# Kernel optimization log

Measured on AMD Instinct MI355X. Metric: run time of the kernel, lower is better.

The kernel has to match this reference:

```python
import jax, jax.numpy as jnp
import numpy as np

NUM_HEADS = 8
D_CONV = 4
NORMALIZER = 16.0
LN_EPS = 1e-5


def setup_inputs() -> dict:
    key = jax.random.key(0)
    ks = jax.random.split(key, 9)
    B, L, E = 4, 2048, 1024
    dk = E // 2
    return {
        "x": jax.random.normal(ks[0], (B, L, E), jnp.float32),
        "conv_w": jax.random.normal(ks[1], (E, D_CONV), jnp.float32) * 0.3,
        "wq": jax.random.normal(ks[2], (E, dk), jnp.float32) * 0.02,
        "wkg": jax.random.normal(ks[3], (E, dk), jnp.float32) * 0.02,
        "wv": jax.random.normal(ks[4], (E, E), jnp.float32) * 0.02,
        "wg": jax.random.normal(ks[5], (E, E), jnp.float32) * 0.02,
        "bg": jax.random.normal(ks[6], (E,), jnp.float32) * 0.02,
        "wout": jax.random.normal(ks[7], (E, E), jnp.float32) * 0.02,
        "aug_balance": jax.random.normal(ks[8], (dk,), jnp.float32) * 0.1,
    }


def _causal_dwconv_silu(x, w):
    # x: [B, L, E]; w: [E, W] depthwise kernel. Causal: left-pad W-1 zeros.
    xt = jnp.transpose(x, (0, 2, 1))  # [B, E, L]
    y = jax.lax.conv_general_dilated(
        xt, w[:, None, :], window_strides=(1,), padding=[(w.shape[1] - 1, 0)],
        feature_group_count=x.shape[-1], dimension_numbers=("NCH", "OIH", "NCH"))
    return jnp.transpose(jax.nn.silu(y), (0, 2, 1))  # [B, L, E]


def _gla(q, k, v, gk, scale):
    # Gated linear attention recurrence (fused_chunk_gla math):
    #   S_t = S_{t-1} * exp(gk_t)[:, None] + k_t (outer) v_t
    #   o_t = (scale * q_t) @ S_t
    # q, k, gk: [B,H,L,Dk]; v: [B,H,L,Dv]
    B, H, L, Dk = q.shape
    Dv = v.shape[-1]

    def step(S, inp):
        qt, kt, vt, gt = inp  # [B,H,Dk], [B,H,Dk], [B,H,Dv], [B,H,Dk]
        S = S * jnp.exp(gt)[..., None] + kt[..., None] * vt[..., None, :]
        ot = jnp.einsum("bhk,bhkv->bhv", qt * scale, S)
        return S, ot

    mv = lambda a: jnp.moveaxis(a, 2, 0)  # L to leading axis for scan
    S0 = jnp.zeros((B, H, Dk, Dv), q.dtype)
    _, o = jax.lax.scan(step, S0, (mv(q), mv(k), mv(v), mv(gk)))
    return jnp.moveaxis(o, 0, 2)  # [B,H,L,Dv]


def reference(x, conv_w, wq, wkg, wv, wg, bg, wout, aug_balance):
    B, L, E = x.shape
    H = NUM_HEADS
    xc = _causal_dwconv_silu(x, conv_w)
    q = xc @ wq            # [B,L,dk]
    kg = xc @ wkg          # [B,L,dk]
    v = xc @ wv            # [B,L,E]
    g = xc @ wg + bg       # [B,L,E]

    gk = jax.nn.log_sigmoid(kg) / NORMALIZER
    k = 1.0 - jnp.exp(gk)

    dkh = q.shape[-1] // H  # key_dim per head
    to_heads = lambda t: t.reshape(B, L, H, -1).transpose(0, 2, 1, 3)
    qh, kh, vh, gkh = to_heads(q), to_heads(k), to_heads(v), to_heads(gk)

    scale = dkh ** -0.5
    o = _gla(qh, kh, vh, gkh, scale)  # [B,H,L,head_dim]

    # Augmented term: aug_w[b,h,l] = sum_d q[b,h,l,d] * aug[h,d] * k[b,h,l,d]
    aug = aug_balance.reshape(H, dkh)
    aug_w = jnp.einsum("bhld,hd,bhld->bhl", qh, aug, kh)
    o = o + jax.nn.sigmoid(aug_w[..., None] * vh)

    # LayerNorm over head_dim, no affine
    mu = o.mean(-1, keepdims=True)
    var = o.var(-1, keepdims=True)
    o = (o - mu) * jax.lax.rsqrt(var + LN_EPS)

    o = o.transpose(0, 2, 1, 3).reshape(B, L, E)
    return (jax.nn.silu(g) * o) @ wout
```

## Files before the change

### kernel.cpp

```cpp
#include <hip/hip_runtime.h>
#include <stdint.h>

typedef unsigned short u16;
typedef unsigned int u32;
typedef __attribute__((ext_vector_type(4))) float f32x4;
typedef __attribute__((ext_vector_type(8))) short short8;
typedef __attribute__((ext_vector_type(8))) _Float16 f16x8;

#define H 8
#define LSEQ 2048
#define E 1024
#define DK 512
#define DVH 128
#define DKH 64
#define NCHUNK 32
#define MROWS 8192
#define LN_EPS 1e-5f

static __device__ __forceinline__ float bf2f(u16 u) {
    union { float f; u32 i; } v; v.i = ((u32)u) << 16; return v.f;
}
static __device__ __forceinline__ u16 f2bf(float f) {
    union { float f; u32 i; } v; v.f = f;
    u32 r = v.i + 0x7FFFu + ((v.i >> 16) & 1u);
    return (u16)(r >> 16);
}

__global__ __launch_bounds__(256) void k_conv(const float* __restrict__ x,
                                              const float* __restrict__ cw,
                                              u16* __restrict__ xc) {
    const int l0 = blockIdx.x * 64;
    const int c  = blockIdx.y * 256 + threadIdx.x;
    const int b  = blockIdx.z;
    const f32x4 w = *(const f32x4*)(cw + c * 4);
    const float* base = x + (size_t)b * LSEQ * E + c;
    u16* ob = xc + (size_t)b * LSEQ * E + c;
    float x3 = (l0 >= 3) ? base[(size_t)(l0 - 3) * E] : 0.f;
    float x2 = (l0 >= 2) ? base[(size_t)(l0 - 2) * E] : 0.f;
    float x1 = (l0 >= 1) ? base[(size_t)(l0 - 1) * E] : 0.f;
#pragma unroll 8
    for (int r = 0; r < 64; r++) {
        const float x0 = base[(size_t)(l0 + r) * E];
        float a = x3 * w[0];
        a = fmaf(x2, w[1], a);
        a = fmaf(x1, w[2], a);
        a = fmaf(x0, w[3], a);
        const float s = a / (1.f + __expf(-a));
        ob[(size_t)(l0 + r) * E] = f2bf(s);
        x3 = x2; x2 = x1; x1 = x0;
    }
}

__global__ __launch_bounds__(256) void k_transpose_all(const float* __restrict__ wq,
                                                       const float* __restrict__ wkg,
                                                       const float* __restrict__ wv,
                                                       const float* __restrict__ wg,
                                                       const float* __restrict__ wout,
                                                       u16* __restrict__ wcat,
                                                       u16* __restrict__ woutT) {
    __shared__ float tile[32][33];
    const int z = blockIdx.z;
    const float* src; u16* dst; int Ncols;
    if (z == 0)      { src = wq;   dst = wcat;                        Ncols = 512; }
    else if (z == 1) { src = wkg;  dst = wcat + (size_t)512 * 1024;   Ncols = 512; }
    else if (z == 2) { src = wv;   dst = wcat + (size_t)1024 * 1024;  Ncols = 1024; }
    else if (z == 3) { src = wg;   dst = wcat + (size_t)2048 * 1024;  Ncols = 1024; }
    else             { src = wout; dst = woutT;                       Ncols = 1024; }
    const int n0 = blockIdx.x * 32, k0 = blockIdx.y * 32;
    if (n0 >= Ncols) return;
    const int K = 1024;
    const int tx = threadIdx.x & 31, ty = threadIdx.x >> 5;
#pragma unroll
    for (int p = 0; p < 4; p++) {
        const int r = p * 8 + ty;
        tile[r][tx] = src[(size_t)(k0 + r) * Ncols + n0 + tx];
    }
    __syncthreads();
#pragma unroll
    for (int p = 0; p < 4; p++) {
        const int rn = p * 8 + ty;
        dst[(size_t)(n0 + rn) * K + k0 + tx] = f2bf(tile[tx][rn]);
    }
}

__global__ __launch_bounds__(512, 1) void k_gemm0(const u16* __restrict__ A,
                                                  const u16* __restrict__ Bt,
                                                  u16* __restrict__ oQ, u16* __restrict__ oKG,
                                                  u16* __restrict__ oV, u16* __restrict__ oSG,
                                                  const float* __restrict__ bg) {
    const int K = 1024;
    __shared__ __align__(16) u16 smem[3][16384];
    const int tid = threadIdx.x;
    const int lane = tid & 63, wv = tid >> 6;
    const int wm = wv >> 2, wn = wv & 3;

    const int id = blockIdx.x;
    const int local = id >> 3;
    const int bx = ((id & 7) << 2) | (local & 3);
    const int by = local >> 2;

    const size_t rowBase = (size_t)bx * 256;
    const size_t colBase = (size_t)by * 256;

    auto stage = [&](int hh, int sl) {
        u16* slotA = &smem[sl][0];
        u16* slotB = &smem[sl][8192];
        const u16* gA = A + rowBase * K + hh * 32;
        const u16* gB = Bt + colBase * K + hh * 32;
#pragma unroll
        for (int i = 0; i < 2; i++) {
            const int u = i * 512 + wv * 64 + lane;
            const int row = u >> 2;
            const int sg = (lane & 3) ^ ((row >> 1) & 3);
            __builtin_amdgcn_global_load_lds(
                (const __attribute__((address_space(1))) void*)(gA + (size_t)row * K + sg * 8),
                (__attribute__((address_space(3))) void*)(slotA + (i * 512 + wv * 64) * 8), 16, 0, 0);
        }
#pragma unroll
        for (int i = 0; i < 2; i++) {
            const int u = i * 512 + wv * 64 + lane;
            const int row = u >> 2;
            const int sg = (lane & 3) ^ ((row >> 1) & 3);
            __builtin_amdgcn_global_load_lds(
                (const __attribute__((address_space(1))) void*)(gB + (size_t)row * K + sg * 8),
                (__attribute__((address_space(3))) void*)(slotB + (i * 512 + wv * 64) * 8), 16, 0, 0);
        }
    };

    f32x4 acc[8][4];
#pragma unroll
    for (int m = 0; m < 8; m++)
#pragma unroll
        for (int n = 0; n < 4; n++) acc[m][n] = (f32x4){0.f, 0.f, 0.f, 0.f};

    const int rsub = lane & 15;
    const int cgl = lane >> 4;

    stage(0, 0); stage(1, 1);

    const int NT2 = K >> 5;
    int sl = 0;
    for (int h = 0; h < NT2; h++) {
        if (h + 1 < NT2) asm volatile("s_waitcnt vmcnt(4)" ::: "memory");
        else             asm volatile("s_waitcnt vmcnt(0)" ::: "memory");
        asm volatile("s_barrier" ::: "memory");
        const u16* As = &smem[sl][0];
        const u16* Bs = &smem[sl][8192];
        short8 bfr[4];
#pragma unroll
        for (int ni = 0; ni < 4; ni++) {
            const int row = wn * 64 + ni * 16 + rsub;
            const int g = cgl ^ ((row >> 1) & 3);
            bfr[ni] = *(const short8*)(Bs + row * 32 + g * 8);
        }
        if (h + 2 < NT2) stage(h + 2, (sl + 2) % 3);
        __builtin_amdgcn_s_setprio(1);
#pragma unroll
        for (int mi = 0; mi < 8; mi++) {
            const int row = wm * 128 + mi * 16 + rsub;
            const int g = cgl ^ ((row >> 1) & 3);
            const short8 af = *(const short8*)(As + row * 32 + g * 8);
#pragma unroll
            for (int ni = 0; ni < 4; ni++)
                acc[mi][ni] = __builtin_amdgcn_mfma_f32_16x16x32_bf16(af, bfr[ni], acc[mi][ni], 0, 0, 0);
        }
        __builtin_amdgcn_s_setprio(0);
        sl = (sl + 1) % 3;
    }

    const int r0 = (lane >> 4) * 4;
    u16* lds = &smem[0][0];
    const int cbase = (int)colBase;
    u16* seg; int stride; int c0;
    if (cbase < 512)       { seg = oQ;  stride = 512;  c0 = cbase; }
    else if (cbase < 1024) { seg = oKG; stride = 512;  c0 = cbase - 512; }
    else if (cbase < 2048) { seg = oV;  stride = 1024; c0 = cbase - 1024; }
    else                   { seg = oSG; stride = 1024; c0 = cbase - 2048; }
    const bool isSG = (cbase >= 2048);
#pragma unroll
    for (int p = 0; p < 2; p++) {
        asm volatile("s_barrier" ::: "memory");
        if (wm == p) {
#pragma unroll
            for (int ni = 0; ni < 4; ni++) {
                const int lcol = wn * 64 + ni * 16 + rsub;
                const float bgv = isSG ? bg[cbase - 2048 + lcol] : 0.f;
#pragma unroll
                for (int mi = 0; mi < 8; mi++) {
#pragma unroll
                    for (int r = 0; r < 4; r++) {
                        const int lrow = mi * 16 + r0 + r;
                        float val = acc[mi][ni][r];
                        if (isSG) { const float y = val + bgv; val = y / (1.f + __expf(-y)); }
                        lds[lrow * 256 + lcol] = f2bf(val);
                    }
                }
            }
        }
        asm volatile("s_barrier" ::: "memory");
#pragma unroll
        for (int i = 0; i < 8; i++) {
            const int unit = i * 512 + tid;
            const int row = unit >> 5, u = unit & 31;
            const uint4 vv = *(const uint4*)(lds + row * 256 + u * 8);
            *(uint4*)(seg + (rowBase + p * 128 + row) * (size_t)stride + c0 + u * 8) = vv;
        }
    }
}

__global__ __launch_bounds__(512, 1) void k_gemm1(const u16* __restrict__ A,
                                                  const u16* __restrict__ Bt,
                                                  float* __restrict__ oF) {
    const int K = 1024, N = 1024;
    __shared__ __align__(16) u16 smem[4][12288];
    const int tid = threadIdx.x;
    const int lane = tid & 63, wv = tid >> 6;
    const int wm = wv >> 1, wn = wv & 1;

    const int id = blockIdx.y * gridDim.x + blockIdx.x;
    const int bx = ((id & 7) << 2) | ((id >> 3) & 3);
    const int by = id >> 5;

    const size_t rowBase = (size_t)bx * 256;
    const size_t colBase = (size_t)by * 128;

    auto stageA = [&](int hh) {
        u16* slotA = &smem[hh & 3][0];
        const u16* g = A + rowBase * K + hh * 32;
#pragma unroll
        for (int i = 0; i < 2; i++) {
            const int r = i * 128 + wv * 16 + (lane >> 2);
            const int sg = (lane & 3) ^ ((r >> 1) & 3);
            __builtin_amdgcn_global_load_lds(
                (const __attribute__((address_space(1))) void*)(g + (size_t)r * K + sg * 8),
                (__attribute__((address_space(3))) void*)(slotA + i * 4096 + wv * 512), 16, 0, 0);
        }
    };
    auto stageB = [&](int hh) {
        u16* slotB = &smem[hh & 3][8192];
        const u16* g = Bt + colBase * K + hh * 32;
        const int r = wv * 16 + (lane >> 2);
        const int sg = (lane & 3) ^ ((r >> 1) & 3);
        __builtin_amdgcn_global_load_lds(
            (const __attribute__((address_space(1))) void*)(g + (size_t)r * K + sg * 8),
            (__attribute__((address_space(3))) void*)(slotB + wv * 512), 16, 0, 0);
    };

    f32x4 acc[4][4];
#pragma unroll
    for (int m = 0; m < 4; m++)
#pragma unroll
        for (int n = 0; n < 4; n++) acc[m][n] = (f32x4){0.f, 0.f, 0.f, 0.f};

    const int rsub = lane & 15;
    const int cgl = lane >> 4;

    stageA(0); stageB(0);
    stageA(1); stageB(1);
    stageA(2); stageB(2);

    const int NT2 = K >> 5;
    for (int h = 0; h < NT2; h++) {
        const int rem = NT2 - 1 - h;
        if (rem >= 2)      asm volatile("s_waitcnt vmcnt(6)" ::: "memory");
        else if (rem == 1) asm volatile("s_waitcnt vmcnt(3)" ::: "memory");
        else               asm volatile("s_waitcnt vmcnt(0)" ::: "memory");
        asm volatile("s_barrier" ::: "memory");
        const u16* As = &smem[h & 3][0];
        const u16* Bs = As + 8192;
        short8 af[4], bfr[4];
#pragma unroll
        for (int mi = 0; mi < 4; mi++) {
            const int row = wm * 64 + mi * 16 + rsub;
            const int g = cgl ^ ((row >> 1) & 3);
            af[mi] = *(const short8*)(As + row * 32 + g * 8);
        }
#pragma unroll
        for (int ni = 0; ni < 4; ni++) {
            const int row = wn * 64 + ni * 16 + rsub;
            const int g = cgl ^ ((row >> 1) & 3);
            bfr[ni] = *(const short8*)(Bs + row * 32 + g * 8);
        }
        if (h + 3 < NT2) { stageA(h + 3); stageB(h + 3); }
        __builtin_amdgcn_s_setprio(1);
#pragma unroll
        for (int mi = 0; mi < 4; mi++)
#pragma unroll
            for (int ni = 0; ni < 4; ni++)
                acc[mi][ni] = __builtin_amdgcn_mfma_f32_16x16x32_bf16(af[mi], bfr[ni], acc[mi][ni], 0, 0, 0);
        __builtin_amdgcn_s_setprio(0);
    }

    const int r0 = (lane >> 4) * 4;
#pragma unroll
    for (int mi = 0; mi < 4; mi++)
#pragma unroll
        for (int ni = 0; ni < 4; ni++) {
            const size_t col = colBase + wn * 64 + ni * 16 + rsub;
#pragma unroll
            for (int r = 0; r < 4; r++) {
                const size_t row = rowBase + wm * 64 + mi * 16 + r0 + r;
                oF[row * (size_t)N + col] = acc[mi][ni][r];
            }
        }
}

__global__ __launch_bounds__(256) void k_gla1(const u16* __restrict__ q,
                                              const u16* __restrict__ kg,
                                              const u16* __restrict__ v,
                                              const float* __restrict__ aug,
                                              u16* __restrict__ qt,
                                              u16* __restrict__ obuf,
                                              float* __restrict__ Sd,
                                              float* __restrict__ Dc,
                                              float* __restrict__ augw) {
    __shared__ __align__(16) float    s_f[64][68];
    __shared__ __align__(16) _Float16 s_q[64][72];
    __shared__ __align__(16) _Float16 s_k[64][72];
    __shared__ __align__(16) _Float16 s_kT[64][72];
    __shared__ __align__(16) _Float16 s_a[64][72];
    __shared__ __align__(16) _Float16 s_vT[128][72];
    const int c = blockIdx.x, bh = blockIdx.y;
    const int b = bh >> 3, h = bh & 7;
    const int tid = threadIdx.x;
    const size_t rowBase = (size_t)b * LSEQ + c * 64;
    const size_t sdBase = (size_t)bh * NCHUNK + c;

    const int tA = tid >> 2, g4 = tid & 3;
    uint4 qr0, qr1;
    {
        const int d0 = g4 * 16;
        const u16* kp = kg + (rowBase + tA) * DK + h * 64 + d0;
        const uint4 k0 = *(const uint4*)kp;
        const uint4 k1 = *(const uint4*)(kp + 8);
        const u16 kv[16] = {
            (u16)(k0.x & 0xffff), (u16)(k0.x >> 16), (u16)(k0.y & 0xffff), (u16)(k0.y >> 16),
            (u16)(k0.z & 0xffff), (u16)(k0.z >> 16), (u16)(k0.w & 0xffff), (u16)(k0.w >> 16),
            (u16)(k1.x & 0xffff), (u16)(k1.x >> 16), (u16)(k1.y & 0xffff), (u16)(k1.y >> 16),
            (u16)(k1.z & 0xffff), (u16)(k1.z >> 16), (u16)(k1.w & 0xffff), (u16)(k1.w >> 16) };
#pragma unroll
        for (int j = 0; j < 16; j++) {
            const float xk = bf2f(kv[j]);
            const float ls = fminf(xk, 0.f) - __logf(1.f + __expf(-fabsf(xk)));
            s_f[tA][d0 + j] = ls * (1.f / 16.f);
        }
        const u16* qp = q + (rowBase + tA) * DK + h * 64 + d0;
        qr0 = *(const uint4*)qp;
        qr1 = *(const uint4*)(qp + 8);

        const int dv0 = g4 * 32;
        const u16* vp = v + (rowBase + tA) * E + h * 128 + dv0;
#pragma unroll
        for (int j8 = 0; j8 < 32; j8 += 8) {
            const uint4 u = *(const uint4*)(vp + j8);
            s_vT[dv0 + j8 + 0][tA] = (_Float16)bf2f((u16)(u.x & 0xffff));
            s_vT[dv0 + j8 + 1][tA] = (_Float16)bf2f((u16)(u.x >> 16));
            s_vT[dv0 + j8 + 2][tA] = (_Float16)bf2f((u16)(u.y & 0xffff));
            s_vT[dv0 + j8 + 3][tA] = (_Float16)bf2f((u16)(u.y >> 16));
            s_vT[dv0 + j8 + 4][tA] = (_Float16)bf2f((u16)(u.z & 0xffff));
            s_vT[dv0 + j8 + 5][tA] = (_Float16)bf2f((u16)(u.z >> 16));
            s_vT[dv0 + j8 + 6][tA] = (_Float16)bf2f((u16)(u.w & 0xffff));
            s_vT[dv0 + j8 + 7][tA] = (_Float16)bf2f((u16)(u.w >> 16));
        }
    }
    __syncthreads();

    {
        const int d = tid >> 2, qseg = tid & 3;
        float part = 0.f;
#pragma unroll
        for (int j = 0; j < 16; j++) part += s_f[qseg * 16 + j][d];
        float incl = part;
        const float u1 = __shfl_up(incl, 1, 4); if (qseg >= 1) incl += u1;
        const float u2 = __shfl_up(incl, 2, 4); if (qseg >= 2) incl += u2;
        float run = incl - part;
#pragma unroll
        for (int j = 0; j < 16; j++) {
            const int t = qseg * 16 + j;
            const float g = s_f[t][d];
            run += g;
            const float kk = 1.f - __expf(g);
            const float ktil = kk * __expf(-run);
            s_k[t][d] = (_Float16)ktil;
            s_kT[d][t] = (_Float16)ktil;
            s_a[t][d] = (_Float16)kk;
            s_f[t][d] = run;
        }
    }
    __syncthreads();

    {
        const int t = tA, d0 = g4 * 16;
        const u16 qv16[16] = {
            (u16)(qr0.x & 0xffff), (u16)(qr0.x >> 16), (u16)(qr0.y & 0xffff), (u16)(qr0.y >> 16),
            (u16)(qr0.z & 0xffff), (u16)(qr0.z >> 16), (u16)(qr0.w & 0xffff), (u16)(qr0.w >> 16),
            (u16)(qr1.x & 0xffff), (u16)(qr1.x >> 16), (u16)(qr1.y & 0xffff), (u16)(qr1.y >> 16),
            (u16)(qr1.z & 0xffff), (u16)(qr1.z >> 16), (u16)(qr1.w & 0xffff), (u16)(qr1.w >> 16) };
        float qv[16];
        float augp = 0.f;
#pragma unroll
        for (int j = 0; j < 16; j++) {
            const int d = d0 + j;
            const float qraw = bf2f(qv16[j]);
            const float L = s_f[t][d];
            const float kk = (float)s_a[t][d];
            const float qtv = qraw * __expf(L) * 0.125f;
            s_q[t][d] = (_Float16)qtv;
            qv[j] = qtv;
            augp = fmaf(qraw * aug[h * 64 + d], kk, augp);
        }
        u16* qto = qt + (rowBase + t) * DK + h * 64 + d0;
#pragma unroll
        for (int j8 = 0; j8 < 16; j8 += 8) {
            uint4 u;
            u.x = (u32)f2bf(qv[j8 + 0]) | ((u32)f2bf(qv[j8 + 1]) << 16);
            u.y = (u32)f2bf(qv[j8 + 2]) | ((u32)f2bf(qv[j8 + 3]) << 16);
            u.z = (u32)f2bf(qv[j8 + 4]) | ((u32)f2bf(qv[j8 + 5]) << 16);
            u.w = (u32)f2bf(qv[j8 + 6]) | ((u32)f2bf(qv[j8 + 7]) << 16);
            *(uint4*)(qto + j8) = u;
        }
        augp += __shfl_xor(augp, 1);
        augp += __shfl_xor(augp, 2);
        if ((tid & 3) == 0) augw[(size_t)bh * LSEQ + c * 64 + t] = augp;
    }
    __syncthreads();

    const int wv = tid >> 6, lane = tid & 63;
    const int rsub = lane & 15, kq8 = (lane >> 4) * 8, r0 = (lane >> 4) * 4;
    {
#pragma unroll
        for (int si = 0; si < 4; si++) {
            if (si <= wv) {
                f32x4 acc = (f32x4){0.f, 0.f, 0.f, 0.f};
#pragma unroll
                for (int kk = 0; kk < 2; kk++) {
                    const f16x8 af = *(const f16x8*)&s_q[wv * 16 + rsub][kk * 32 + kq8];
                    const f16x8 bf = *(const f16x8*)&s_k[si * 16 + rsub][kk * 32 + kq8];
                    acc = __builtin_amdgcn_mfma_f32_16x16x32_f16(af, bf, acc, 0, 0, 0);
                }
                const int scol = si * 16 + rsub;
#pragma unroll
                for (int r = 0; r < 4; r++) {
                    const int trow = wv * 16 + r0 + r;
                    const float val = (scol <= trow) ? acc[r] : 0.f;
                    s_a[trow][scol] = (_Float16)val;
                }
            } else {
#pragma unroll
                for (int r = 0; r < 4; r++)
                    s_a[wv * 16 + r0 + r][si * 16 + rsub] = (_Float16)0.f;
            }
        }
    }
    __syncthreads();

    {
        f32x4 oacc[8];
#pragma unroll
        for (int n = 0; n < 8; n++) oacc[n] = (f32x4){0.f, 0.f, 0.f, 0.f};
        const f16x8 a0 = *(const f16x8*)&s_a[wv * 16 + rsub][kq8];
        const f16x8 a1 = *(const f16x8*)&s_a[wv * 16 + rsub][32 + kq8];
#pragma unroll
        for (int n = 0; n < 8; n++) {
            const f16x8 b0 = *(const f16x8*)&s_vT[n * 16 + rsub][kq8];
            const f16x8 b1 = *(const f16x8*)&s_vT[n * 16 + rsub][32 + kq8];
            oacc[n] = __builtin_amdgcn_mfma_f32_16x16x32_f16(a0, b0, oacc[n], 0, 0, 0);
            oacc[n] = __builtin_amdgcn_mfma_f32_16x16x32_f16(a1, b1, oacc[n], 0, 0, 0);
        }
        u16* ob = obuf + ((size_t)bh * LSEQ + c * 64) * DVH;
#pragma unroll
        for (int n = 0; n < 8; n++) {
            const int dv = n * 16 + rsub;
#pragma unroll
            for (int r = 0; r < 4; r++) {
                const int trow = wv * 16 + r0 + r;
                ob[(size_t)trow * DVH + dv] = f2bf(oacc[n][r]);
            }
        }
    }

    {
        f32x4 sacc[8];
#pragma unroll
        for (int n = 0; n < 8; n++) sacc[n] = (f32x4){0.f, 0.f, 0.f, 0.f};
        const f16x8 a0 = *(const f16x8*)&s_kT[wv * 16 + rsub][kq8];
        const f16x8 a1 = *(const f16x8*)&s_kT[wv * 16 + rsub][32 + kq8];
#pragma unroll
        for (int n = 0; n < 8; n++) {
            const f16x8 b0 = *(const f16x8*)&s_vT[n * 16 + rsub][kq8];
            const f16x8 b1 = *(const f16x8*)&s_vT[n * 16 + rsub][32 + kq8];
            sacc[n] = __builtin_amdgcn_mfma_f32_16x16x32_f16(a0, b0, sacc[n], 0, 0, 0);
            sacc[n] = __builtin_amdgcn_mfma_f32_16x16x32_f16(a1, b1, sacc[n], 0, 0, 0);
        }
        float dend[4];
#pragma unroll
        for (int r = 0; r < 4; r++) dend[r] = __expf(s_f[63][wv * 16 + r0 + r]);
#pragma unroll
        for (int n = 0; n < 8; n++) {
            const int dv = n * 16 + rsub;
#pragma unroll
            for (int r = 0; r < 4; r++) {
                const int d = wv * 16 + r0 + r;
                Sd[(sdBase * DKH + d) * DVH + dv] = sacc[n][r] * dend[r];
            }
        }
        if (rsub == 0) {
#pragma unroll
            for (int r = 0; r < 4; r++) {
                const int d = wv * 16 + r0 + r;
                Dc[sdBase * DKH + d] = dend[r];
            }
        }
    }
}

__global__ __launch_bounds__(256) void k_gla2(const float* __restrict__ Sd,
                                              u16* __restrict__ Ss,
                                              const float* __restrict__ Dc) {
    const int cid = blockIdx.x * 256 + threadIdx.x;
    const int bh = cid >> 13;
    const int e = cid & 8191;
    const int d = e >> 7;
    float run = 0.f;
    const size_t base = (size_t)bh * NCHUNK * 8192 + e;
    for (int c = 0; c < NCHUNK; c++) {
        const size_t idx = base + (size_t)c * 8192;
        const float dl = Sd[idx];
        Ss[idx] = f2bf(run);
        run = fmaf(Dc[((size_t)bh * NCHUNK + c) * DKH + d], run, dl);
    }
}

__global__ __launch_bounds__(256) void k_gla3(const u16* __restrict__ qt,
                                              const u16* __restrict__ v,
                                              const u16* __restrict__ sg,
                                              const u16* __restrict__ obuf,
                                              const u16* __restrict__ Ss,
                                              const float* __restrict__ augw,
                                              u16* __restrict__ a2) {
    __shared__ __align__(16) _Float16 s_ST[128][72];
    __shared__ __align__(16) _Float16 s_qr[64][72];
    __shared__ __align__(16) float    s_O2[64][132];
    const int c = blockIdx.x, bh = blockIdx.y;
    const int b = bh >> 3, h = bh & 7;
    const int tid = threadIdx.x;
    const size_t rowBase = (size_t)b * LSEQ + c * 64;
    {
        const int d = tid >> 2, dv0 = (tid & 3) * 32;
        const u16* sp = Ss + (((size_t)bh * NCHUNK + c) * DKH + d) * DVH + dv0;
#pragma unroll
        for (int j8 = 0; j8 < 32; j8 += 8) {
            const uint4 u = *(const uint4*)(sp + j8);
            s_ST[dv0 + j8 + 0][d] = (_Float16)bf2f((u16)(u.x & 0xffff));
            s_ST[dv0 + j8 + 1][d] = (_Float16)bf2f((u16)(u.x >> 16));
            s_ST[dv0 + j8 + 2][d] = (_Float16)bf2f((u16)(u.y & 0xffff));
            s_ST[dv0 + j8 + 3][d] = (_Float16)bf2f((u16)(u.y >> 16));
            s_ST[dv0 + j8 + 4][d] = (_Float16)bf2f((u16)(u.z & 0xffff));
            s_ST[dv0 + j8 + 5][d] = (_Float16)bf2f((u16)(u.z >> 16));
            s_ST[dv0 + j8 + 6][d] = (_Float16)bf2f((u16)(u.w & 0xffff));
            s_ST[dv0 + j8 + 7][d] = (_Float16)bf2f((u16)(u.w >> 16));
        }
    }
    {
        const int t = tid >> 2, d0 = (tid & 3) * 16;
        const u16* qp = qt + (rowBase + t) * DK + h * 64 + d0;
        const uint4 q0 = *(const uint4*)qp;
        const uint4 q1 = *(const uint4*)(qp + 8);
        const u16 qv[16] = {
            (u16)(q0.x & 0xffff), (u16)(q0.x >> 16), (u16)(q0.y & 0xffff), (u16)(q0.y >> 16),
            (u16)(q0.z & 0xffff), (u16)(q0.z >> 16), (u16)(q0.w & 0xffff), (u16)(q0.w >> 16),
            (u16)(q1.x & 0xffff), (u16)(q1.x >> 16), (u16)(q1.y & 0xffff), (u16)(q1.y >> 16),
            (u16)(q1.z & 0xffff), (u16)(q1.z >> 16), (u16)(q1.w & 0xffff), (u16)(q1.w >> 16) };
#pragma unroll
        for (int j = 0; j < 16; j++) s_qr[t][d0 + j] = (_Float16)bf2f(qv[j]);
    }
    __syncthreads();
    {
        const int wv = tid >> 6, lane = tid & 63;
        const int rsub = lane & 15, kq8 = (lane >> 4) * 8, r0 = (lane >> 4) * 4;
        const f16x8 a0 = *(const f16x8*)&s_qr[wv * 16 + rsub][kq8];
        const f16x8 a1 = *(const f16x8*)&s_qr[wv * 16 + rsub][32 + kq8];
#pragma unroll
        for (int n = 0; n < 8; n++) {
            f32x4 acc = (f32x4){0.f, 0.f, 0.f, 0.f};
            const f16x8 b0 = *(const f16x8*)&s_ST[n * 16 + rsub][kq8];
            const f16x8 b1 = *(const f16x8*)&s_ST[n * 16 + rsub][32 + kq8];
            acc = __builtin_amdgcn_mfma_f32_16x16x32_f16(a0, b0, acc, 0, 0, 0);
            acc = __builtin_amdgcn_mfma_f32_16x16x32_f16(a1, b1, acc, 0, 0, 0);
            const int dv = n * 16 + rsub;
#pragma unroll
            for (int r = 0; r < 4; r++) s_O2[wv * 16 + r0 + r][dv] = acc[r];
        }
    }
    __syncthreads();
    const int t = tid >> 2, dv0 = (tid & 3) * 32;
    float o[32];
    const u16* op = obuf + ((size_t)bh * LSEQ + c * 64 + t) * DVH + dv0;
#pragma unroll
    for (int j8 = 0; j8 < 32; j8 += 8) {
        const uint4 u = *(const uint4*)(op + j8);
        o[j8 + 0] = bf2f((u16)(u.x & 0xffff)); o[j8 + 1] = bf2f((u16)(u.x >> 16));
        o[j8 + 2] = bf2f((u16)(u.y & 0xffff)); o[j8 + 3] = bf2f((u16)(u.y >> 16));
        o[j8 + 4] = bf2f((u16)(u.z & 0xffff)); o[j8 + 5] = bf2f((u16)(u.z >> 16));
        o[j8 + 6] = bf2f((u16)(u.w & 0xffff)); o[j8 + 7] = bf2f((u16)(u.w >> 16));
    }
#pragma unroll
    for (int j = 0; j < 32; j += 4) {
        const f32x4 sv = *(const f32x4*)&s_O2[t][dv0 + j];
        o[j + 0] += sv[0]; o[j + 1] += sv[1]; o[j + 2] += sv[2]; o[j + 3] += sv[3];
    }
    const float aw = augw[(size_t)bh * LSEQ + c * 64 + t];
    const u16* vp = v + (rowBase + t) * E + h * 128 + dv0;
#pragma unroll
    for (int j8 = 0; j8 < 32; j8 += 8) {
        const uint4 u = *(const uint4*)(vp + j8);
        const float vv[8] = {
            bf2f((u16)(u.x & 0xffff)), bf2f((u16)(u.x >> 16)),
            bf2f((u16)(u.y & 0xffff)), bf2f((u16)(u.y >> 16)),
            bf2f((u16)(u.z & 0xffff)), bf2f((u16)(u.z >> 16)),
            bf2f((u16)(u.w & 0xffff)), bf2f((u16)(u.w >> 16)) };
#pragma unroll
        for (int j = 0; j < 8; j++)
            o[j8 + j] += 1.f / (1.f + __expf(-aw * vv[j]));
    }
    float sum = 0.f;
#pragma unroll
    for (int j = 0; j < 32; j++) sum += o[j];
    sum += __shfl_xor(sum, 1); sum += __shfl_xor(sum, 2);
    const float mu = sum * (1.f / 128.f);
    float sq = 0.f;
#pragma unroll
    for (int j = 0; j < 32; j++) { const float dlt = o[j] - mu; sq = fmaf(dlt, dlt, sq); }
    sq += __shfl_xor(sq, 1); sq += __shfl_xor(sq, 2);
    const float rs = rsqrtf(sq * (1.f / 128.f) + LN_EPS);
    const u16* sp2 = sg + (rowBase + t) * E + h * 128 + dv0;
    u16* ap = a2 + (rowBase + t) * E + h * 128 + dv0;
#pragma unroll
    for (int j8 = 0; j8 < 32; j8 += 8) {
        const uint4 us = *(const uint4*)(sp2 + j8);
        const float sv[8] = {
            bf2f((u16)(us.x & 0xffff)), bf2f((u16)(us.x >> 16)),
            bf2f((u16)(us.y & 0xffff)), bf2f((u16)(us.y >> 16)),
            bf2f((u16)(us.z & 0xffff)), bf2f((u16)(us.z >> 16)),
            bf2f((u16)(us.w & 0xffff)), bf2f((u16)(us.w >> 16)) };
        uint4 u;
        u.x = (u32)f2bf(sv[0] * ((o[j8 + 0] - mu) * rs)) | ((u32)f2bf(sv[1] * ((o[j8 + 1] - mu) * rs)) << 16);
        u.y = (u32)f2bf(sv[2] * ((o[j8 + 2] - mu) * rs)) | ((u32)f2bf(sv[3] * ((o[j8 + 3] - mu) * rs)) << 16);
        u.z = (u32)f2bf(sv[4] * ((o[j8 + 4] - mu) * rs)) | ((u32)f2bf(sv[5] * ((o[j8 + 5] - mu) * rs)) << 16);
        u.w = (u32)f2bf(sv[6] * ((o[j8 + 6] - mu) * rs)) | ((u32)f2bf(sv[7] * ((o[j8 + 7] - mu) * rs)) << 16);
        *(uint4*)(ap + j8) = u;
    }
}

extern "C" void kernel_launch(void* const* d_in, const int* in_sizes, int n_in,
                              void* d_out, int out_size, void* d_ws, size_t ws_size,
                              hipStream_t stream) {
    const float* x      = (const float*)d_in[0];
    const float* conv_w = (const float*)d_in[1];
    const float* wq     = (const float*)d_in[2];
    const float* wkg    = (const float*)d_in[3];
    const float* wv     = (const float*)d_in[4];
    const float* wg     = (const float*)d_in[5];
    const float* bg     = (const float*)d_in[6];
    const float* wout   = (const float*)d_in[7];
    const float* aug    = (const float*)d_in[8];

    char* ws = (char*)d_ws;
    size_t off = 0;
    auto alloc = [&](size_t bytes) -> char* {
        char* p = ws + off;
        off += (bytes + 255) & ~(size_t)255;
        return p;
    };
    u16* xc    = (u16*)alloc((size_t)MROWS * E * 2);
    u16* wcat  = (u16*)alloc((size_t)3072 * E * 2);
    u16* woutT = (u16*)alloc((size_t)E * E * 2);
    u16* qb    = (u16*)alloc((size_t)MROWS * DK * 2);
    u16* kgb   = (u16*)alloc((size_t)MROWS * DK * 2);
    u16* vb    = (u16*)alloc((size_t)MROWS * E * 2);
    u16* sgb   = (u16*)alloc((size_t)MROWS * E * 2);
    u16* qtb   = (u16*)alloc((size_t)MROWS * DK * 2);
    u16* obuf  = (u16*)alloc((size_t)32 * LSEQ * DVH * 2);
    u16* Ssb   = (u16*)alloc((size_t)32 * NCHUNK * DKH * DVH * 2);
    float* Dc  = (float*)alloc((size_t)32 * NCHUNK * DKH * 4);
    float* augw= (float*)alloc((size_t)32 * LSEQ * 4);
    u16* a2    = qb;
    float* Sd  = (float*)d_out;

    k_conv<<<dim3(LSEQ / 64, E / 256, 4), 256, 0, stream>>>(x, conv_w, xc);
    k_transpose_all<<<dim3(32, 32, 5), 256, 0, stream>>>(wq, wkg, wv, wg, wout, wcat, woutT);
    k_gemm0<<<384, 512, 0, stream>>>(xc, wcat, qb, kgb, vb, sgb, bg);
    k_gla1<<<dim3(NCHUNK, 32), 256, 0, stream>>>(qb, kgb, vb, aug, qtb, obuf, Sd, Dc, augw);
    k_gla2<<<1024, 256, 0, stream>>>(Sd, Ssb, Dc);
    k_gla3<<<dim3(NCHUNK, 32), 256, 0, stream>>>(qtb, vb, sgb, obuf, Ssb, augw, a2);
    k_gemm1<<<dim3(32, 8), 512, 0, stream>>>(a2, woutT, (float*)d_out);
}
```

Measured before the change: 171.7 us.

## Restructure projection GEMM mainloop to 64-wide K tiles with double-buffered chunk staging

The fused projection GEMM now stages 64-wide K tiles split into four 128-row chunks (two for A, two for B) in a double buffer, instead of a triple buffer of 32-wide tiles. It uses a new XOR swizzle over eight 16-byte groups, and each warp's 128-row A slice is processed as two 64-row halves. Loads for the next tile are issued in the middle of compute on the current one, with barriers around each MFMA burst. The goal is to halve the number of outer iterations and wait points, interleaving global-to-LDS copies with MFMA work. The cost is more barriers per iteration and a full vmcnt(0) wait each K step, which could expose memory latency.

```diff
diff --git a/kernel.cpp b/kernel.cpp
--- a/kernel.cpp
+++ b/kernel.cpp
@@ -16,6 +16,9 @@
 #define NCHUNK 32
 #define MROWS 8192
 #define LN_EPS 1e-5f
+
+#define AS1 __attribute__((address_space(1)))
+#define AS3 __attribute__((address_space(3)))
 
 static __device__ __forceinline__ float bf2f(u16 u) {
     union { float f; u32 i; } v; v.i = ((u32)u) << 16; return v.f;
@@ -89,7 +92,7 @@
                                                   u16* __restrict__ oV, u16* __restrict__ oSG,
                                                   const float* __restrict__ bg) {
     const int K = 1024;
-    __shared__ __align__(16) u16 smem[3][16384];
+    __shared__ __align__(16) u16 smem[8][8192];
     const int tid = threadIdx.x;
     const int lane = tid & 63, wv = tid >> 6;
     const int wm = wv >> 2, wn = wv & 3;
@@ -102,28 +105,20 @@
     const size_t rowBase = (size_t)bx * 256;
     const size_t colBase = (size_t)by * 256;
 
-    auto stage = [&](int hh, int sl) {
-        u16* slotA = &smem[sl][0];
-        u16* slotB = &smem[sl][8192];
-        const u16* gA = A + rowBase * K + hh * 32;
-        const u16* gB = Bt + colBase * K + hh * 32;
+    auto stageChunk = [&](int kt, int c) {
+        const int slot = ((kt & 1) << 2) | c;
+        u16* dstBase = &smem[slot][0];
+        const u16* gsrc = (c < 2)
+            ? (A + (rowBase + (size_t)c * 128) * K + kt * 64)
+            : (Bt + (colBase + (size_t)(c - 2) * 128) * K + kt * 64);
 #pragma unroll
         for (int i = 0; i < 2; i++) {
             const int u = i * 512 + wv * 64 + lane;
-            const int row = u >> 2;
-            const int sg = (lane & 3) ^ ((row >> 1) & 3);
+            const int row = u >> 3, g = u & 7;
+            const int sg = g ^ (row & 7);
             __builtin_amdgcn_global_load_lds(
-                (const __attribute__((address_space(1))) void*)(gA + (size_t)row * K + sg * 8),
-                (__attribute__((address_space(3))) void*)(slotA + (i * 512 + wv * 64) * 8), 16, 0, 0);
-        }
-#pragma unroll
-        for (int i = 0; i < 2; i++) {
-            const int u = i * 512 + wv * 64 + lane;
-            const int row = u >> 2;
-            const int sg = (lane & 3) ^ ((row >> 1) & 3);
-            __builtin_amdgcn_global_load_lds(
-                (const __attribute__((address_space(1))) void*)(gB + (size_t)row * K + sg * 8),
-                (__attribute__((address_space(3))) void*)(slotB + (i * 512 + wv * 64) * 8), 16, 0, 0);
+                (const AS1 void*)(gsrc + (size_t)row * K + sg * 8),
+                (AS3 void*)(dstBase + (i * 512 + wv * 64) * 8), 16, 0, 0);
         }
     };
 
@@ -135,37 +130,52 @@
 
     const int rsub = lane & 15;
     const int cgl = lane >> 4;
-
-    stage(0, 0); stage(1, 1);
-
-    const int NT2 = K >> 5;
-    int sl = 0;
-    for (int h = 0; h < NT2; h++) {
-        if (h + 1 < NT2) asm volatile("s_waitcnt vmcnt(4)" ::: "memory");
-        else             asm volatile("s_waitcnt vmcnt(0)" ::: "memory");
+    const int brow0 = (wn & 1) * 64;
+
+    stageChunk(0, 0); stageChunk(0, 1); stageChunk(0, 2); stageChunk(0, 3);
+
+    for (int kt = 0; kt < 16; kt++) {
+        asm volatile("s_waitcnt vmcnt(0)" ::: "memory");
         asm volatile("s_barrier" ::: "memory");
-        const u16* As = &smem[sl][0];
-        const u16* Bs = &smem[sl][8192];
-        short8 bfr[4];
-#pragma unroll
-        for (int ni = 0; ni < 4; ni++) {
-            const int row = wn * 64 + ni * 16 + rsub;
-            const int g = cgl ^ ((row >> 1) & 3);
-            bfr[ni] = *(const short8*)(Bs + row * 32 + g * 8);
-        }
-        if (h + 2 < NT2) stage(h + 2, (sl + 2) % 3);
-        __builtin_amdgcn_s_setprio(1);
-#pragma unroll
-        for (int mi = 0; mi < 8; mi++) {
-            const int row = wm * 128 + mi * 16 + rsub;
-            const int g = cgl ^ ((row >> 1) & 3);
-            const short8 af = *(const short8*)(As + row * 32 + g * 8);
-#pragma unroll
-            for (int ni = 0; ni < 4; ni++)
-                acc[mi][ni] = __builtin_amdgcn_mfma_f32_16x16x32_bf16(af, bfr[ni], acc[mi][ni], 0, 0, 0);
-        }
-        __builtin_amdgcn_s_setprio(0);
-        sl = (sl + 1) % 3;
+        const u16* Ac = &smem[((kt & 1) << 2) | wm][0];
+        const u16* Bc = &smem[((kt & 1) << 2) | 2 | (wn >> 1)][0];
+        short8 bf[4][2];
+#pragma unroll
+        for (int t = 0; t < 2; t++) {
+#pragma unroll
+            for (int x = 0; x < 2; x++) {
+                short8 af[4];
+#pragma unroll
+                for (int mi = 0; mi < 4; mi++) {
+                    const int rowp = x * 64 + mi * 16 + rsub;
+                    const int g = (t * 4 + cgl) ^ (rowp & 7);
+                    af[mi] = *(const short8*)(Ac + rowp * 64 + g * 8);
+                }
+                if (x == 0) {
+#pragma unroll
+                    for (int ni = 0; ni < 4; ni++) {
+                        const int rowp = brow0 + ni * 16 + rsub;
+                        const int g = (t * 4 + cgl) ^ (rowp & 7);
+                        bf[ni][t] = *(const short8*)(Bc + rowp * 64 + g * 8);
+                    }
+                }
+                if (kt < 15 && t == 0) {
+                    if (x == 0) { stageChunk(kt + 1, 0); stageChunk(kt + 1, 1); }
+                    else        { stageChunk(kt + 1, 2); stageChunk(kt + 1, 3); }
+                }
+                asm volatile("s_barrier" ::: "memory");
+                asm volatile("s_waitcnt lgkmcnt(0)" ::: "memory");
+                __builtin_amdgcn_s_setprio(1);
+#pragma unroll
+                for (int mi = 0; mi < 4; mi++)
+#pragma unroll
+                    for (int ni = 0; ni < 4; ni++)
+                        acc[x * 4 + mi][ni] = __builtin_amdgcn_mfma_f32_16x16x32_bf16(
+                            af[mi], bf[ni][t], acc[x * 4 + mi][ni], 0, 0, 0);
+                __builtin_amdgcn_s_setprio(0);
+                asm volatile("s_barrier" ::: "memory");
+            }
+        }
     }
 
     const int r0 = (lane >> 4) * 4;
@@ -186,11 +196,11 @@
                 const int lcol = wn * 64 + ni * 16 + rsub;
                 const float bgv = isSG ? bg[cbase - 2048 + lcol] : 0.f;
 #pragma unroll
-                for (int mi = 0; mi < 8; mi++) {
+                for (int ai = 0; ai < 8; ai++) {
 #pragma unroll
                     for (int r = 0; r < 4; r++) {
-                        const int lrow = mi * 16 + r0 + r;
-                        float val = acc[mi][ni][r];
+                        const int lrow = (ai >> 2) * 64 + (ai & 3) * 16 + r0 + r;
+                        float val = acc[ai][ni][r];
                         if (isSG) { const float y = val + bgv; val = y / (1.f + __expf(-y)); }
                         lds[lrow * 256 + lcol] = f2bf(val);
                     }
@@ -232,8 +242,8 @@
             const int r = i * 128 + wv * 16 + (lane >> 2);
             const int sg = (lane & 3) ^ ((r >> 1) & 3);
             __builtin_amdgcn_global_load_lds(
-                (const __attribute__((address_space(1))) void*)(g + (size_t)r * K + sg * 8),
-                (__attribute__((address_space(3))) void*)(slotA + i * 4096 + wv * 512), 16, 0, 0);
+                (const AS1 void*)(g + (size_t)r * K + sg * 8),
+                (AS3 void*)(slotA + i * 4096 + wv * 512), 16, 0, 0);
         }
     };
     auto stageB = [&](int hh) {
@@ -242,8 +252,8 @@
         const int r = wv * 16 + (lane >> 2);
         const int sg = (lane & 3) ^ ((r >> 1) & 3);
         __builtin_amdgcn_global_load_lds(
-            (const __attribute__((address_space(1))) void*)(g + (size_t)r * K + sg * 8),
-            (__attribute__((address_space(3))) void*)(slotB + wv * 512), 16, 0, 0);
+            (const AS1 void*)(g + (size_t)r * K + sg * 8),
+            (AS3 void*)(slotB + wv * 512), 16, 0, 0);
     };
 
     f32x4 acc[4][4];
```

After: 176.2 us. 1.03x slower.
